# Performance work log

Hardware: AMD Instinct MI355X
Metric: run time of the kernel (lower is better)

Reference implementation:

```python
import jax, jax.numpy as jnp
import numpy as np

N_NODES = 50000
N_EDGES = 150000
NODE_F, EDGE_F = 4, 11
HID, HID_OUT = 512, 1024
VS, AS_, N_ACT = 2048, 2048, 1000


def _graph_conv(x, W, b, src, dst, n, edge_weight=None):
    # DGL GraphConv, norm='both': D_out^{-1/2} on src feats, sum-aggregate, D_in^{-1/2} on dst.
    deg_out = jnp.maximum(jnp.zeros((n,), x.dtype).at[src].add(1.0), 1.0)
    deg_in = jnp.maximum(jnp.zeros((n,), x.dtype).at[dst].add(1.0), 1.0)
    h = x * (deg_out[:, None] ** -0.5)
    mult_first = W.shape[0] > W.shape[1]
    if mult_first:
        h = h @ W
    m = h[src]  # [E, d] gather
    if edge_weight is not None:
        m = m * edge_weight  # elementwise u_mul_e
    agg = jax.ops.segment_sum(m, dst, num_segments=n)
    if not mult_first:
        agg = agg @ W
    return agg * (deg_in[:, None] ** -0.5) + b


def setup_inputs() -> dict:
    key = jax.random.key(0)
    ks = jax.random.split(key, 16)
    s = 0.05
    return {
        'node_feats': jax.random.normal(ks[0], (N_NODES, NODE_F), jnp.float32),
        'edge_feats': jax.random.normal(ks[1], (N_EDGES, EDGE_F), jnp.float32),
        'W1': jax.random.normal(ks[2], (NODE_F, EDGE_F), jnp.float32) * s,
        'b1': jnp.zeros((EDGE_F,), jnp.float32),
        'W2': jax.random.normal(ks[3], (EDGE_F, HID), jnp.float32) * s,
        'b2': jnp.zeros((HID,), jnp.float32),
        'W3': jax.random.normal(ks[4], (HID, HID_OUT), jnp.float32) * s,
        'b3': jnp.zeros((HID_OUT,), jnp.float32),
        'Wv1': jax.random.normal(ks[5], (HID_OUT, VS), jnp.float32) * s,
        'bv1': jnp.zeros((VS,), jnp.float32),
        'Wv2': jax.random.normal(ks[6], (VS, 1), jnp.float32) * s,
        'bv2': jnp.zeros((1,), jnp.float32),
        'Wa1': jax.random.normal(ks[7], (HID_OUT, AS_), jnp.float32) * s,
        'ba1': jnp.zeros((AS_,), jnp.float32),
        'Wa2': jax.random.normal(ks[8], (AS_, N_ACT), jnp.float32) * s,
        'ba2': jnp.zeros((N_ACT,), jnp.float32),
        'src': jax.random.randint(ks[9], (N_EDGES,), 0, N_NODES, jnp.int32),
        'dst': jax.random.randint(ks[10], (N_EDGES,), 0, N_NODES, jnp.int32),
    }


def reference(node_feats, edge_feats, W1, b1, W2, b2, W3, b3,
              Wv1, bv1, Wv2, bv2, Wa1, ba1, Wa2, ba2, src, dst):
    n = node_feats.shape[0]
    loop = jnp.arange(n, dtype=src.dtype)
    srcL = jnp.concatenate([src, loop])  # add_self_loop
    dstL = jnp.concatenate([dst, loop])
    # self-loop edges get zero edge features (DGL default)
    ef = jnp.concatenate([edge_feats, jnp.zeros((n, edge_feats.shape[1]), edge_feats.dtype)], axis=0)

    h = jax.nn.relu(_graph_conv(node_feats, W1, b1, srcL, dstL, n))          # [N, 11]
    h = jax.nn.relu(_graph_conv(h, W2, b2, srcL, dstL, n, edge_weight=ef))   # [N, 512]
    h = _graph_conv(h, W3, b3, srcL, dstL, n)                                # [N, 1024]

    g_emb = jnp.mean(h, axis=0, keepdims=True)  # dgl.mean_nodes, single graph -> [1, 1024]

    v = jax.nn.relu(g_emb @ Wv1 + bv1) @ Wv2 + bv2        # [1, 1]
    a = jax.nn.relu(g_emb @ Wa1 + ba1) @ Wa2 + ba2        # [1, N_ACT]
    return v + (a - a.mean())
```

## Files before the change

### kernel.cpp

```cpp
#include <hip/hip_runtime.h>

#define NN 50000
#define NE 150000
#define NB 196

__global__ __launch_bounds__(256) void k_deg(const int* __restrict__ src,
                                             const int* __restrict__ dst,
                                             int* __restrict__ deg_out,
                                             int* __restrict__ deg_in) {
    int e = blockIdx.x * 256 + threadIdx.x;
    if (e < NE) {
        atomicAdd(&deg_out[src[e]], 1);
        atomicAdd(&deg_in[dst[e]], 1);
    }
}

__global__ __launch_bounds__(256) void k_bsum(const int* __restrict__ deg_in,
                                              const int* __restrict__ deg_out,
                                              int* __restrict__ bsum_in,
                                              int* __restrict__ bsum_out) {
    __shared__ int si[256], so[256];
    int t = threadIdx.x;
    int idx = blockIdx.x * 256 + t;
    si[t] = (idx < NN) ? deg_in[idx] : 0;
    so[t] = (idx < NN) ? deg_out[idx] : 0;
    __syncthreads();
    for (int off = 128; off >= 1; off >>= 1) {
        if (t < off) { si[t] += si[t + off]; so[t] += so[t + off]; }
        __syncthreads();
    }
    if (t == 0) { bsum_in[blockIdx.x] = si[0]; bsum_out[blockIdx.x] = so[0]; }
}

__global__ __launch_bounds__(256) void k_rowptr(const int* __restrict__ deg_in,
                                                const int* __restrict__ deg_out,
                                                const int* __restrict__ bsum_in,
                                                const int* __restrict__ bsum_out,
                                                const float* __restrict__ x,
                                                int* __restrict__ rp_in,
                                                int* __restrict__ rp_out,
                                                float* __restrict__ dins,
                                                float* __restrict__ douts,
                                                float4* __restrict__ xs4) {
    __shared__ int si[256], so[256];
    int b = blockIdx.x, t = threadIdx.x;
    si[t] = (t < b) ? bsum_in[t] : 0;
    so[t] = (t < b) ? bsum_out[t] : 0;
    __syncthreads();
    for (int off = 128; off >= 1; off >>= 1) {
        if (t < off) { si[t] += si[t + off]; so[t] += so[t + off]; }
        __syncthreads();
    }
    int off_in = si[0], off_out = so[0];
    __syncthreads();
    int idx = b * 256 + t;
    int di = (idx < NN) ? deg_in[idx] : 0;
    int dq = (idx < NN) ? deg_out[idx] : 0;
    si[t] = di; so[t] = dq;
    __syncthreads();
    for (int off = 1; off < 256; off <<= 1) {
        int a = (t >= off) ? si[t - off] : 0;
        int c2 = (t >= off) ? so[t - off] : 0;
        __syncthreads();
        si[t] += a; so[t] += c2;
        __syncthreads();
    }
    if (idx < NN) {
        rp_in[idx]  = off_in  + si[t] - di;
        rp_out[idx] = off_out + so[t] - dq;
        float dif = rsqrtf((float)(di + 1));
        float dqf = rsqrtf((float)(dq + 1));
        dins[idx] = dif;
        douts[idx] = dqf;
        float4 x4 = ((const float4*)x)[idx];
        x4.x *= dqf; x4.y *= dqf; x4.z *= dqf; x4.w *= dqf;
        xs4[idx] = x4;
    }
    if (b == 0 && t == 0) { rp_in[NN] = NE; rp_out[NN] = NE; }
}

__global__ __launch_bounds__(256) void k_scatter(const int* __restrict__ src,
                                                 const int* __restrict__ dst,
                                                 const int* __restrict__ rp_in,
                                                 const int* __restrict__ rp_out,
                                                 int* __restrict__ cur_in,
                                                 int* __restrict__ cur_out,
                                                 int2* __restrict__ ei_pack,
                                                 int* __restrict__ nbr_out) {
    int e = blockIdx.x * 256 + threadIdx.x;
    if (e >= NE) return;
    int s = src[e], d = dst[e];
    int pi = rp_in[d] + atomicAdd(&cur_in[d], 1);
    ei_pack[pi] = make_int2(e, s);
    int po = rp_out[s] + atomicAdd(&cur_out[s], 1);
    nbr_out[po] = d;
}

__global__ __launch_bounds__(256) void k_conv1g(const float4* __restrict__ xs4,
                                                const int2* __restrict__ ei_pack,
                                                const int* __restrict__ rp_in,
                                                const int* __restrict__ nbr_out,
                                                const int* __restrict__ rp_out,
                                                const float* __restrict__ dins,
                                                const float* __restrict__ douts,
                                                const float* __restrict__ W1,
                                                const float* __restrict__ b1,
                                                float* __restrict__ h1s,
                                                float* __restrict__ c) {
    int n = blockIdx.x * 256 + threadIdx.x;
    if (n >= NN) return;
    float din  = dins[n];
    float dout = douts[n];
    float4 a = xs4[n];
    int beg = rp_in[n], end = rp_in[n + 1];
    for (int p = beg; p < end; p++) {
        int s = ei_pack[p].y;
        float4 xs = xs4[s];
        a.x += xs.x; a.y += xs.y; a.z += xs.z; a.w += xs.w;
    }
    float cacc = din;
    int ob = rp_out[n], oe = rp_out[n + 1];
    for (int p = ob; p < oe; p++)
        cacc += dins[nbr_out[p]];
    c[n] = cacc;
    #pragma unroll
    for (int j = 0; j < 11; j++) {
        float y = a.x * W1[0 * 11 + j] + a.y * W1[1 * 11 + j] +
                  a.z * W1[2 * 11 + j] + a.w * W1[3 * 11 + j];
        y = fmaxf(fmaf(y, din, b1[j]), 0.f);
        h1s[n * 11 + j] = y * dout;
    }
}

#define G2 32
__global__ __launch_bounds__(512) void k_conv2f(const float* __restrict__ h1s,
                                                const float* __restrict__ ef,
                                                const int2* __restrict__ ei_pack,
                                                const int* __restrict__ rp_in,
                                                const float* __restrict__ c,
                                                const float* __restrict__ dins,
                                                const float* __restrict__ douts,
                                                const float* __restrict__ W2,
                                                const float* __restrict__ b2,
                                                float* __restrict__ t) {
    __shared__ float tile[G2 * 11];
    __shared__ float din_sh[G2], w_sh[G2];
    int n0 = blockIdx.x * G2;
    int tid = threadIdx.x;
    if (tid < G2 * 11) {
        int i = tid / 11, j = tid % 11;
        int n = n0 + i;
        float acc = 0.f;
        if (n < NN) {
            int beg = rp_in[n], end = rp_in[n + 1];
            for (int p = beg; p < end; p++) {
                int2 es = ei_pack[p];
                acc = fmaf(h1s[es.y * 11 + j], ef[es.x * 11 + j], acc);
            }
        }
        tile[tid] = acc;
    } else if (tid >= 512 - G2) {
        int i = tid - (512 - G2);
        int n = n0 + i;
        if (n < NN) {
            din_sh[i] = dins[n];
            w_sh[i]   = c[n] * douts[n] * (1.0f / NN);
        } else { din_sh[i] = 0.f; w_sh[i] = 0.f; }
    }
    __syncthreads();
    float w[11];
    #pragma unroll
    for (int j = 0; j < 11; j++) w[j] = W2[j * 512 + tid];
    float bias = b2[tid];
    float acc = 0.f;
    for (int i = 0; i < G2; i++) {
        float dot = 0.f;
        #pragma unroll
        for (int j = 0; j < 11; j++) dot = fmaf(tile[i * 11 + j], w[j], dot);
        float y = fmaxf(fmaf(dot, din_sh[i], bias), 0.f);
        acc = fmaf(w_sh[i], y, acc);
    }
    atomicAdd(&t[tid], acc);
}

__global__ __launch_bounds__(256) void k_g(const float* __restrict__ t,
                                           const float* __restrict__ W3,
                                           const float* __restrict__ b3,
                                           float* __restrict__ g) {
    int b = blockIdx.x;
    int oc = b & 3, kc = b >> 2;
    int o = oc * 256 + threadIdx.x;
    int k0 = kc * 16;
    __shared__ float ts[16];
    if (threadIdx.x < 16) ts[threadIdx.x] = t[k0 + threadIdx.x];
    __syncthreads();
    float acc = (kc == 0) ? b3[o] : 0.f;
    #pragma unroll
    for (int k = 0; k < 16; k++) acc = fmaf(ts[k], W3[(size_t)(k0 + k) * 1024 + o], acc);
    atomicAdd(&g[o], acc);
}

__global__ __launch_bounds__(256) void k_heads1(const float* __restrict__ g,
                                                const float* __restrict__ Wv1,
                                                const float* __restrict__ Wa1,
                                                float* __restrict__ hv_raw,
                                                float* __restrict__ ha_raw) {
    int b = blockIdx.x;
    int oc = b >> 5, kc = b & 31;
    int idx = oc * 256 + threadIdx.x;
    int k0 = kc * 32;
    __shared__ float gs[32];
    if (threadIdx.x < 32) gs[threadIdx.x] = g[k0 + threadIdx.x];
    __syncthreads();
    const float* W; float* outp; int o;
    if (idx < 2048) { W = Wv1; outp = hv_raw; o = idx; }
    else            { W = Wa1; outp = ha_raw; o = idx - 2048; }
    float acc = 0.f;
    #pragma unroll 8
    for (int k = 0; k < 32; k++) acc = fmaf(gs[k], W[(size_t)(k0 + k) * 2048 + o], acc);
    atomicAdd(&outp[o], acc);
}

__global__ __launch_bounds__(256) void k_heads2(const float* __restrict__ hv_raw,
                                                const float* __restrict__ bv1,
                                                const float* __restrict__ ha_raw,
                                                const float* __restrict__ ba1,
                                                const float* __restrict__ Wv2,
                                                const float* __restrict__ bv2,
                                                const float* __restrict__ Wa2,
                                                float* __restrict__ a_acc,
                                                float* __restrict__ v) {
    int b = blockIdx.x;
    int tid = threadIdx.x;
    if (b < 256) {
        int oc = b >> 6, kc = b & 63;
        int k0 = kc * 32;
        __shared__ float hs[32];
        if (tid < 32) hs[tid] = fmaxf(ha_raw[k0 + tid] + ba1[k0 + tid], 0.f);
        __syncthreads();
        int o = oc * 256 + tid;
        if (o < 1000) {
            float acc = 0.f;
            #pragma unroll 8
            for (int k = 0; k < 32; k++)
                acc = fmaf(hs[k], Wa2[(size_t)(k0 + k) * 1000 + o], acc);
            atomicAdd(&a_acc[o], acc);
        }
    } else {
        __shared__ float red[256];
        float acc = 0.f;
        for (int k = tid; k < 2048; k += 256)
            acc = fmaf(fmaxf(hv_raw[k] + bv1[k], 0.f), Wv2[k], acc);
        red[tid] = acc;
        __syncthreads();
        for (int s = 128; s >= 1; s >>= 1) {
            if (tid < s) red[tid] += red[tid + s];
            __syncthreads();
        }
        if (tid == 0) *v = red[0] + bv2[0];
    }
}

__global__ __launch_bounds__(1024) void k_final(const float* __restrict__ a_acc,
                                                const float* __restrict__ ba2,
                                                const float* __restrict__ vptr,
                                                float* __restrict__ out) {
    __shared__ float red[1024];
    int tid = threadIdx.x;
    float ai = (tid < 1000) ? a_acc[tid] + ba2[tid] : 0.f;
    red[tid] = ai;
    __syncthreads();
    for (int s = 512; s >= 1; s >>= 1) {
        if (tid < s) red[tid] += red[tid + s];
        __syncthreads();
    }
    float amean = red[0] * (1.0f / 1000.0f);
    if (tid < 1000) out[tid] = vptr[0] + ai - amean;
}

extern "C" void kernel_launch(void* const* d_in, const int* in_sizes, int n_in,
                              void* d_out, int out_size, void* d_ws, size_t ws_size,
                              hipStream_t stream) {
    const float* x   = (const float*)d_in[0];
    const float* ef  = (const float*)d_in[1];
    const float* W1  = (const float*)d_in[2];
    const float* b1  = (const float*)d_in[3];
    const float* W2  = (const float*)d_in[4];
    const float* b2  = (const float*)d_in[5];
    const float* W3  = (const float*)d_in[6];
    const float* b3  = (const float*)d_in[7];
    const float* Wv1 = (const float*)d_in[8];
    const float* bv1 = (const float*)d_in[9];
    const float* Wv2 = (const float*)d_in[10];
    const float* bv2 = (const float*)d_in[11];
    const float* Wa1 = (const float*)d_in[12];
    const float* ba1 = (const float*)d_in[13];
    const float* Wa2 = (const float*)d_in[14];
    const float* ba2 = (const float*)d_in[15];
    const int*   src = (const int*)d_in[16];
    const int*   dst = (const int*)d_in[17];
    float* out = (float*)d_out;

    char* ws = (char*)d_ws;
    size_t off = 0;
    auto alloc = [&](size_t bytes) -> void* {
        void* p = ws + off;
        off = (off + bytes + 255) & ~(size_t)255;
        return p;
    };
    int*   deg_out = (int*)  alloc(NN * 4);
    int*   deg_in  = (int*)  alloc(NN * 4);
    int*   cur_in  = (int*)  alloc(NN * 4);
    int*   cur_out = (int*)  alloc(NN * 4);
    float* t       = (float*)alloc(512 * 4);
    float* g       = (float*)alloc(1024 * 4);
    float* hv_raw  = (float*)alloc(2048 * 4);
    float* ha_raw  = (float*)alloc(2048 * 4);
    float* a_acc   = (float*)alloc(1024 * 4);
    size_t zero_bytes = off;
    int*    bsum_in  = (int*)   alloc(NB * 4);
    int*    bsum_out = (int*)   alloc(NB * 4);
    int*    rp_in    = (int*)   alloc((NN + 1) * 4);
    int*    rp_out   = (int*)   alloc((NN + 1) * 4);
    float*  dins     = (float*) alloc(NN * 4);
    float*  douts    = (float*) alloc(NN * 4);
    float4* xs4      = (float4*)alloc((size_t)NN * 16);
    int2*   ei_pack  = (int2*)  alloc((size_t)NE * 8);
    int*    nbr_out  = (int*)   alloc((size_t)NE * 4);
    float*  c        = (float*) alloc(NN * 4);
    float*  h1s      = (float*) alloc((size_t)NN * 11 * 4);
    float*  v        = (float*) alloc(256);

    hipMemsetAsync(d_ws, 0, zero_bytes, stream);

    k_deg<<<(NE + 255) / 256, 256, 0, stream>>>(src, dst, deg_out, deg_in);
    k_bsum<<<NB, 256, 0, stream>>>(deg_in, deg_out, bsum_in, bsum_out);
    k_rowptr<<<NB, 256, 0, stream>>>(deg_in, deg_out, bsum_in, bsum_out, x,
                                     rp_in, rp_out, dins, douts, xs4);
    k_scatter<<<(NE + 255) / 256, 256, 0, stream>>>(src, dst, rp_in, rp_out,
                                                    cur_in, cur_out, ei_pack, nbr_out);
    k_conv1g<<<(NN + 255) / 256, 256, 0, stream>>>(xs4, ei_pack, rp_in, nbr_out, rp_out,
                                                   dins, douts, W1, b1, h1s, c);
    k_conv2f<<<(NN + G2 - 1) / G2, 512, 0, stream>>>(h1s, ef, ei_pack, rp_in, c,
                                                     dins, douts, W2, b2, t);
    k_g<<<128, 256, 0, stream>>>(t, W3, b3, g);
    k_heads1<<<512, 256, 0, stream>>>(g, Wv1, Wa1, hv_raw, ha_raw);
    k_heads2<<<257, 256, 0, stream>>>(hv_raw, bv1, ha_raw, ba1, Wv2, bv2, Wa2, a_acc, v);
    k_final<<<1, 1024, 0, stream>>>(a_acc, ba2, v, out);
}
```

Baseline: 214.5 us.

## Pre-permute edge features into CSR order and parallelize conv2 aggregation over edges

The scatter kernel now copies each edge's 11 features into a 12-float padded buffer in destination-sorted CSR order. The h1 node features are also padded to 12 floats so they can be read as float4. In conv2, each block covers 64 nodes and its threads stride over the block's whole edge range. Each thread finds its destination row by binary search over the shared row pointers and accumulates into the shared tile with LDS atomics. This replaces the old scheme of one thread per node-feature pair serially walking that node's edges with scalar gathers, which suffered load imbalance and uncoalesced access. The cost is extra work in scatter to permute the edge features, more memory traffic from the padding, and contention on the shared atomics.

```diff
diff --git a/kernel.cpp b/kernel.cpp
--- a/kernel.cpp
+++ b/kernel.cpp
@@ -81,23 +81,29 @@
 
 __global__ __launch_bounds__(256) void k_scatter(const int* __restrict__ src,
                                                  const int* __restrict__ dst,
+                                                 const float* __restrict__ ef,
                                                  const int* __restrict__ rp_in,
                                                  const int* __restrict__ rp_out,
                                                  int* __restrict__ cur_in,
                                                  int* __restrict__ cur_out,
-                                                 int2* __restrict__ ei_pack,
+                                                 int* __restrict__ nbr_in,
+                                                 float4* __restrict__ ef4,
                                                  int* __restrict__ nbr_out) {
     int e = blockIdx.x * 256 + threadIdx.x;
     if (e >= NE) return;
     int s = src[e], d = dst[e];
     int pi = rp_in[d] + atomicAdd(&cur_in[d], 1);
-    ei_pack[pi] = make_int2(e, s);
+    nbr_in[pi] = s;
+    const float* er = ef + (size_t)e * 11;
+    ef4[(size_t)pi * 3 + 0] = make_float4(er[0], er[1], er[2], er[3]);
+    ef4[(size_t)pi * 3 + 1] = make_float4(er[4], er[5], er[6], er[7]);
+    ef4[(size_t)pi * 3 + 2] = make_float4(er[8], er[9], er[10], 0.f);
     int po = rp_out[s] + atomicAdd(&cur_out[s], 1);
     nbr_out[po] = d;
 }
 
 __global__ __launch_bounds__(256) void k_conv1g(const float4* __restrict__ xs4,
-                                                const int2* __restrict__ ei_pack,
+                                                const int* __restrict__ nbr_in,
                                                 const int* __restrict__ rp_in,
                                                 const int* __restrict__ nbr_out,
                                                 const int* __restrict__ rp_out,
@@ -105,7 +111,7 @@
                                                 const float* __restrict__ douts,
                                                 const float* __restrict__ W1,
                                                 const float* __restrict__ b1,
-                                                float* __restrict__ h1s,
+                                                float4* __restrict__ h1s4,
                                                 float* __restrict__ c) {
     int n = blockIdx.x * 256 + threadIdx.x;
     if (n >= NN) return;
@@ -114,8 +120,7 @@
     float4 a = xs4[n];
     int beg = rp_in[n], end = rp_in[n + 1];
     for (int p = beg; p < end; p++) {
-        int s = ei_pack[p].y;
-        float4 xs = xs4[s];
+        float4 xs = xs4[nbr_in[p]];
         a.x += xs.x; a.y += xs.y; a.z += xs.z; a.w += xs.w;
     }
     float cacc = din;
@@ -123,19 +128,23 @@
     for (int p = ob; p < oe; p++)
         cacc += dins[nbr_out[p]];
     c[n] = cacc;
+    float y[12];
     #pragma unroll
     for (int j = 0; j < 11; j++) {
-        float y = a.x * W1[0 * 11 + j] + a.y * W1[1 * 11 + j] +
-                  a.z * W1[2 * 11 + j] + a.w * W1[3 * 11 + j];
-        y = fmaxf(fmaf(y, din, b1[j]), 0.f);
-        h1s[n * 11 + j] = y * dout;
-    }
-}
-
-#define G2 32
-__global__ __launch_bounds__(512) void k_conv2f(const float* __restrict__ h1s,
-                                                const float* __restrict__ ef,
-                                                const int2* __restrict__ ei_pack,
+        float t2 = a.x * W1[0 * 11 + j] + a.y * W1[1 * 11 + j] +
+                   a.z * W1[2 * 11 + j] + a.w * W1[3 * 11 + j];
+        y[j] = fmaxf(fmaf(t2, din, b1[j]), 0.f) * dout;
+    }
+    y[11] = 0.f;
+    h1s4[(size_t)n * 3 + 0] = make_float4(y[0], y[1], y[2],  y[3]);
+    h1s4[(size_t)n * 3 + 1] = make_float4(y[4], y[5], y[6],  y[7]);
+    h1s4[(size_t)n * 3 + 2] = make_float4(y[8], y[9], y[10], y[11]);
+}
+
+#define G2 64
+__global__ __launch_bounds__(512) void k_conv2f(const float4* __restrict__ h1s4,
+                                                const float4* __restrict__ ef4,
+                                                const int* __restrict__ nbr_in,
                                                 const int* __restrict__ rp_in,
                                                 const float* __restrict__ c,
                                                 const float* __restrict__ dins,
@@ -143,29 +152,45 @@
                                                 const float* __restrict__ W2,
                                                 const float* __restrict__ b2,
                                                 float* __restrict__ t) {
-    __shared__ float tile[G2 * 11];
+    __shared__ float tile[G2 * 12];
+    __shared__ int rp_sh[G2 + 1];
     __shared__ float din_sh[G2], w_sh[G2];
+    int tid = threadIdx.x;
     int n0 = blockIdx.x * G2;
-    int tid = threadIdx.x;
-    if (tid < G2 * 11) {
-        int i = tid / 11, j = tid % 11;
-        int n = n0 + i;
-        float acc = 0.f;
-        if (n < NN) {
-            int beg = rp_in[n], end = rp_in[n + 1];
-            for (int p = beg; p < end; p++) {
-                int2 es = ei_pack[p];
-                acc = fmaf(h1s[es.y * 11 + j], ef[es.x * 11 + j], acc);
-            }
-        }
-        tile[tid] = acc;
-    } else if (tid >= 512 - G2) {
-        int i = tid - (512 - G2);
-        int n = n0 + i;
-        if (n < NN) {
-            din_sh[i] = dins[n];
-            w_sh[i]   = c[n] * douts[n] * (1.0f / NN);
-        } else { din_sh[i] = 0.f; w_sh[i] = 0.f; }
+    if (tid <= G2) {
+        int n = n0 + tid;
+        rp_sh[tid] = rp_in[(n > NN) ? NN : n];
+    }
+    for (int i = tid; i < G2 * 12; i += 512) tile[i] = 0.f;
+    if (tid < G2) {
+        int n = n0 + tid;
+        if (n < NN) { din_sh[tid] = dins[n]; w_sh[tid] = c[n] * douts[n] * (1.0f / NN); }
+        else        { din_sh[tid] = 0.f;     w_sh[tid] = 0.f; }
+    }
+    __syncthreads();
+    int pbeg = rp_sh[0], pend = rp_sh[G2];
+    for (int p = pbeg + tid; p < pend; p += 512) {
+        int s = nbr_in[p];
+        float4 ha = h1s4[(size_t)s * 3 + 0];
+        float4 hb = h1s4[(size_t)s * 3 + 1];
+        float4 hc = h1s4[(size_t)s * 3 + 2];
+        float4 ea = ef4[(size_t)p * 3 + 0];
+        float4 eb = ef4[(size_t)p * 3 + 1];
+        float4 ec = ef4[(size_t)p * 3 + 2];
+        int lo = 0, hi = G2;
+        while (hi - lo > 1) { int mid = (lo + hi) >> 1; if (rp_sh[mid] <= p) lo = mid; else hi = mid; }
+        float* row = &tile[lo * 12];
+        atomicAdd(&row[0],  ha.x * ea.x);
+        atomicAdd(&row[1],  ha.y * ea.y);
+        atomicAdd(&row[2],  ha.z * ea.z);
+        atomicAdd(&row[3],  ha.w * ea.w);
+        atomicAdd(&row[4],  hb.x * eb.x);
+        atomicAdd(&row[5],  hb.y * eb.y);
+        atomicAdd(&row[6],  hb.z * eb.z);
+        atomicAdd(&row[7],  hb.w * eb.w);
+        atomicAdd(&row[8],  hc.x * ec.x);
+        atomicAdd(&row[9],  hc.y * ec.y);
+        atomicAdd(&row[10], hc.z * ec.z);
     }
     __syncthreads();
     float w[11];
@@ -174,9 +199,11 @@
     float bias = b2[tid];
     float acc = 0.f;
     for (int i = 0; i < G2; i++) {
-        float dot = 0.f;
-        #pragma unroll
-        for (int j = 0; j < 11; j++) dot = fmaf(tile[i * 11 + j], w[j], dot);
+        const float4* trow = (const float4*)&tile[i * 12];
+        float4 ta = trow[0], tb = trow[1], tc = trow[2];
+        float dot = ta.x * w[0] + ta.y * w[1] + ta.z * w[2] + ta.w * w[3] +
+                    tb.x * w[4] + tb.y * w[5] + tb.z * w[6] + tb.w * w[7] +
+                    tc.x * w[8] + tc.y * w[9] + tc.z * w[10];
         float y = fmaxf(fmaf(dot, din_sh[i], bias), 0.f);
         acc = fmaf(w_sh[i], y, acc);
     }
@@ -325,10 +352,11 @@
     float*  dins     = (float*) alloc(NN * 4);
     float*  douts    = (float*) alloc(NN * 4);
     float4* xs4      = (float4*)alloc((size_t)NN * 16);
-    int2*   ei_pack  = (int2*)  alloc((size_t)NE * 8);
+    int*    nbr_in   = (int*)   alloc((size_t)NE * 4);
     int*    nbr_out  = (int*)   alloc((size_t)NE * 4);
+    float4* ef4      = (float4*)alloc((size_t)NE * 48);
+    float4* h1s4     = (float4*)alloc((size_t)NN * 48);
     float*  c        = (float*) alloc(NN * 4);
-    float*  h1s      = (float*) alloc((size_t)NN * 11 * 4);
     float*  v        = (float*) alloc(256);
 
     hipMemsetAsync(d_ws, 0, zero_bytes, stream);
@@ -337,11 +365,11 @@
     k_bsum<<<NB, 256, 0, stream>>>(deg_in, deg_out, bsum_in, bsum_out);
     k_rowptr<<<NB, 256, 0, stream>>>(deg_in, deg_out, bsum_in, bsum_out, x,
                                      rp_in, rp_out, dins, douts, xs4);
-    k_scatter<<<(NE + 255) / 256, 256, 0, stream>>>(src, dst, rp_in, rp_out,
-                                                    cur_in, cur_out, ei_pack, nbr_out);
-    k_conv1g<<<(NN + 255) / 256, 256, 0, stream>>>(xs4, ei_pack, rp_in, nbr_out, rp_out,
-                                                   dins, douts, W1, b1, h1s, c);
-    k_conv2f<<<(NN + G2 - 1) / G2, 512, 0, stream>>>(h1s, ef, ei_pack, rp_in, c,
+    k_scatter<<<(NE + 255) / 256, 256, 0, stream>>>(src, dst, ef, rp_in, rp_out,
+                                                    cur_in, cur_out, nbr_in, ef4, nbr_out);
+    k_conv1g<<<(NN + 255) / 256, 256, 0, stream>>>(xs4, nbr_in, rp_in, nbr_out, rp_out,
+                                                   dins, douts, W1, b1, h1s4, c);
+    k_conv2f<<<(NN + G2 - 1) / G2, 512, 0, stream>>>(h1s4, ef4, nbr_in, rp_in, c,
                                                      dins, douts, W2, b2, t);
     k_g<<<128, 256, 0, stream>>>(t, W3, b3, g);
     k_heads1<<<512, 256, 0, stream>>>(g, Wv1, Wa1, hv_raw, ha_raw);
```

After: 210.4 us. About the same (-1.9%).
